# Optimization experiments

Hardware: AMD Instinct MI355X
Metric: run time of the kernel (lower is better)

The kernel has to match this reference:

```python
import jax, jax.numpy as jnp
import numpy as np

NUM_ITERS = 3
NUM_CAPSULES = 10
NUM_ROUTES = 1152  # 32*6*6
IN_CH = 16
OUT_CH = 32
BATCH = 128


def _squash(t):
    # Faithful to original squash(tensor) with default dim=1 (the batch axis here).
    n2 = jnp.sum(t * t, axis=1, keepdims=True)
    return (n2 / (1.0 + n2)) * t / jnp.sqrt(n2)


def setup_inputs() -> dict:
    key = jax.random.key(0)
    k1, k2 = jax.random.split(key)
    x = jax.random.normal(k1, (BATCH, NUM_ROUTES, IN_CH), dtype=jnp.float32)
    route_weights = jax.random.normal(
        k2, (NUM_CAPSULES, NUM_ROUTES, IN_CH, OUT_CH), dtype=jnp.float32)
    return {"x": x, "route_weights": route_weights}


def reference(x, route_weights):
    # prediction vectors u_hat: [C, B, R, O]
    pred = jnp.einsum('bri,crio->cbro', x, route_weights)
    logits = jnp.zeros_like(pred)  # [C, B, R, O], matching torch zeros of pred size
    outputs = None
    for i in range(NUM_ITERS):
        # routing_softmax with dim=2 -> softmax over the routes axis
        c = jax.nn.softmax(logits, axis=2)
        s = jnp.sum(c * pred, axis=2, keepdims=True)  # [C, B, 1, O]
        outputs = _squash(s)
        if i != NUM_ITERS - 1:
            # delta logits: [C, B, R, 1], broadcasts over O when added
            logits = logits + jnp.sum(pred * outputs, axis=-1, keepdims=True)
    # match torch output shape [C, B, 1, 1, O]
    return outputs[:, :, :, None, :]
```

## Files before the change

### kernel.cpp

```cpp
#include <hip/hip_runtime.h>
#include <math.h>

#define NB 128
#define NR 1152
#define NC 10
#define NCHK 24

typedef __attribute__((ext_vector_type(8))) short bf16x8;
typedef __attribute__((ext_vector_type(16))) float f32x16;

__device__ __forceinline__ unsigned pk_bf16(float a, float b) {
    unsigned r;
    asm("v_cvt_pk_bf16_f32 %0, %1, %2" : "=v"(r) : "v"(a), "v"(b));
    return r;
}

union UF { uint4 q; unsigned u[4]; bf16x8 v; };

template<int MODE>
__global__ __launch_bounds__(512, 2) void pass_z(const float* __restrict__ x,
                                                 const float* __restrict__ W,
                                                 unsigned* __restrict__ xts,
                                                 unsigned* __restrict__ wts,
                                                 float* __restrict__ oacc,
                                                 float* __restrict__ dout,
                                                 float* __restrict__ sbuf,
                                                 float* __restrict__ zbuf,
                                                 int* __restrict__ cnt)
{
    __shared__ float lds[16384];
    __shared__ int lastFlag;
    const int pb = blockIdx.x;
    const int lin = (pb & 7) * 30 + (pb >> 3);
    const int rch = lin / 10;
    const int c   = lin - rch * 10;
    const int t = threadIdx.x;
    const int w = t >> 6, l = t & 63;
    const int h = w >> 1, bp = w & 1;
    const int lo5 = l & 31, hi1 = l >> 5;
    const int r0 = rch * 48 + h * 12;

    if (MODE >= 1) {
        for (int idx = t; idx < 4096; idx += 512)
            lds[(idx >> 5) * 33 + (idx & 31)] = oacc[(size_t)c * 4096 + idx];
    }
    __syncthreads();

    float ov0[16], ov1[16];
    if (MODE >= 1) {
#pragma unroll
        for (int j = 0; j < 16; ++j) {
            int orow = (j & 3) + 8 * (j >> 2) + 4 * hi1;
            ov0[j] = lds[(bp * 64 + lo5) * 33 + orow];
            ov1[j] = lds[(bp * 64 + 32 + lo5) * 33 + orow];
        }
    }

    f32x16 acc0, acc1, zz;
#pragma unroll
    for (int j = 0; j < 16; ++j) { acc0[j] = 0.f; acc1[j] = 0.f; zz[j] = 0.f; }
    float Z0 = 0.f, Z1 = 0.f;

    const float* wb  = W + ((size_t)(c * NR + r0) * 16 + hi1 * 8) * 32 + lo5;
    const float* xp0 = x + ((size_t)(bp * 64 + lo5) * NR + r0) * 16 + hi1 * 8;
    const float* xp1 = x + ((size_t)(bp * 64 + 32 + lo5) * NR + r0) * 16 + hi1 * 8;
    uint4* xt4 = (uint4*)xts;
    uint4* wt4 = (uint4*)wts;
    const int bq0 = bp * 64 + lo5, bq1 = bq0 + 32;

#pragma unroll 4
    for (int rr = 0; rr < 12; ++rr) {
        UF Ah, Al, Xh0, Xl0, Xh1, Xl1;
        const size_t wrow = (size_t)(c * NR + r0 + rr) * 2;
        if (MODE == 0) {
            float wv[8];
#pragma unroll
            for (int j = 0; j < 8; ++j) wv[j] = wb[(size_t)rr * 512 + j * 32];
#pragma unroll
            for (int j = 0; j < 4; ++j) Ah.u[j] = pk_bf16(wv[2*j], wv[2*j+1]);
#pragma unroll
            for (int j = 0; j < 4; ++j) {
                float g0 = __uint_as_float(Ah.u[j] << 16);
                float g1 = __uint_as_float(Ah.u[j] & 0xffff0000u);
                Al.u[j] = pk_bf16(wv[2*j] - g0, wv[2*j+1] - g1);
            }
            if (bp == 0) {
                wt4[wrow * 64 + l]       = Ah.q;
                wt4[(wrow + 1) * 64 + l] = Al.q;
            }
        } else {
            Ah.q = wt4[wrow * 64 + l];
            Al.q = wt4[(wrow + 1) * 64 + l];
        }
        const size_t rb4 = ((size_t)((r0 + rr) * 2 + hi1) * 2) * 128;
        if (MODE == 0) {
            float4 u0 = *(const float4*)(xp0 + rr * 16);
            float4 u1 = *(const float4*)(xp0 + rr * 16 + 4);
            float4 v0 = *(const float4*)(xp1 + rr * 16);
            float4 v1 = *(const float4*)(xp1 + rr * 16 + 4);
            float xv0[8] = {u0.x,u0.y,u0.z,u0.w, u1.x,u1.y,u1.z,u1.w};
            float xv1[8] = {v0.x,v0.y,v0.z,v0.w, v1.x,v1.y,v1.z,v1.w};
#pragma unroll
            for (int j = 0; j < 4; ++j) Xh0.u[j] = pk_bf16(xv0[2*j], xv0[2*j+1]);
#pragma unroll
            for (int j = 0; j < 4; ++j) {
                float g0 = __uint_as_float(Xh0.u[j] << 16);
                float g1 = __uint_as_float(Xh0.u[j] & 0xffff0000u);
                Xl0.u[j] = pk_bf16(xv0[2*j] - g0, xv0[2*j+1] - g1);
            }
#pragma unroll
            for (int j = 0; j < 4; ++j) Xh1.u[j] = pk_bf16(xv1[2*j], xv1[2*j+1]);
#pragma unroll
            for (int j = 0; j < 4; ++j) {
                float g0 = __uint_as_float(Xh1.u[j] << 16);
                float g1 = __uint_as_float(Xh1.u[j] & 0xffff0000u);
                Xl1.u[j] = pk_bf16(xv1[2*j] - g0, xv1[2*j+1] - g1);
            }
            if (((h * 12 + rr) % 10) == c) {
                xt4[rb4 + bq0]       = Xh0.q;
                xt4[rb4 + 128 + bq0] = Xl0.q;
                xt4[rb4 + bq1]       = Xh1.q;
                xt4[rb4 + 128 + bq1] = Xl1.q;
            }
        } else {
            Xh0.q = xt4[rb4 + bq0];
            Xl0.q = xt4[rb4 + 128 + bq0];
            Xh1.q = xt4[rb4 + bq1];
            Xl1.q = xt4[rb4 + 128 + bq1];
        }

        if (MODE == 0) {
            acc0 = __builtin_amdgcn_mfma_f32_32x32x16_bf16(Ah.v, Xh0.v, acc0, 0, 0, 0);
            acc0 = __builtin_amdgcn_mfma_f32_32x32x16_bf16(Al.v, Xh0.v, acc0, 0, 0, 0);
            acc0 = __builtin_amdgcn_mfma_f32_32x32x16_bf16(Ah.v, Xl0.v, acc0, 0, 0, 0);
            acc1 = __builtin_amdgcn_mfma_f32_32x32x16_bf16(Ah.v, Xh1.v, acc1, 0, 0, 0);
            acc1 = __builtin_amdgcn_mfma_f32_32x32x16_bf16(Al.v, Xh1.v, acc1, 0, 0, 0);
            acc1 = __builtin_amdgcn_mfma_f32_32x32x16_bf16(Ah.v, Xl1.v, acc1, 0, 0, 0);
        } else {
            f32x16 q0, q1;
            q0 = __builtin_amdgcn_mfma_f32_32x32x16_bf16(Ah.v, Xh0.v, zz, 0, 0, 0);
            q1 = __builtin_amdgcn_mfma_f32_32x32x16_bf16(Ah.v, Xh1.v, zz, 0, 0, 0);
            q0 = __builtin_amdgcn_mfma_f32_32x32x16_bf16(Al.v, Xh0.v, q0, 0, 0, 0);
            q1 = __builtin_amdgcn_mfma_f32_32x32x16_bf16(Al.v, Xh1.v, q1, 0, 0, 0);
            q0 = __builtin_amdgcn_mfma_f32_32x32x16_bf16(Ah.v, Xl0.v, q0, 0, 0, 0);
            q1 = __builtin_amdgcn_mfma_f32_32x32x16_bf16(Ah.v, Xl1.v, q1, 0, 0, 0);
            float d0 = 0.f, d1 = 0.f;
#pragma unroll
            for (int j = 0; j < 16; ++j) {
                d0 = fmaf(q0[j], ov0[j], d0);
                d1 = fmaf(q1[j], ov1[j], d1);
            }
            d0 += __shfl_xor(d0, 32);
            d1 += __shfl_xor(d1, 32);
            float e0 = __expf(d0 - 20.0f);
            float e1 = __expf(d1 - 20.0f);
            Z0 += e0; Z1 += e1;
#pragma unroll
            for (int j = 0; j < 16; ++j) {
                acc0[j] = fmaf(e0, q0[j], acc0[j]);
                acc1[j] = fmaf(e1, q1[j], acc1[j]);
            }
        }
    }

    const int b0 = bp * 64 + lo5, b1 = b0 + 32;
    __syncthreads();
#pragma unroll
    for (int j = 0; j < 16; ++j) {
        int orow = (j & 3) + 8 * (j >> 2) + 4 * hi1;
        lds[h * 4096 + b0 * 32 + (orow ^ lo5)] = acc0[j];
        lds[h * 4096 + b1 * 32 + (orow ^ lo5)] = acc1[j];
    }
    __syncthreads();
    float* sc = sbuf + (size_t)c * 4096;
    for (int idx = t; idx < 4096; idx += 512) {
        int b = idx >> 5, o = idx & 31;
        float s = 0.f;
#pragma unroll
        for (int hh = 0; hh < 4; ++hh)
            s += lds[hh * 4096 + b * 32 + (o ^ (b & 31))];
        (void)__hip_atomic_fetch_add(sc + idx, s, __ATOMIC_RELAXED,
                                     __HIP_MEMORY_SCOPE_AGENT);
    }
    if (MODE >= 1) {
        __syncthreads();
        if (l < 32) {
            lds[h * 128 + bp * 64 + lo5] = Z0;
            lds[h * 128 + bp * 64 + 32 + lo5] = Z1;
        }
        __syncthreads();
        if (t < 128) {
            float z = lds[t] + lds[128 + t] + lds[256 + t] + lds[384 + t];
            (void)__hip_atomic_fetch_add(zbuf + (size_t)c * 128 + t, z,
                                         __ATOMIC_RELAXED, __HIP_MEMORY_SCOPE_AGENT);
        }
    }

    __syncthreads();
    if (t == 0) {
        int old = __hip_atomic_fetch_add(&cnt[c], 1,
                                         __ATOMIC_RELAXED, __HIP_MEMORY_SCOPE_AGENT);
        lastFlag = (old == NCHK - 1) ? 1 : 0;
    }
    __syncthreads();
    if (!lastFlag) return;

    if (MODE >= 1) {
        if (t < NB) {
            lds[8192 + t] = __hip_atomic_load(zbuf + (size_t)c * 128 + t,
                                              __ATOMIC_RELAXED, __HIP_MEMORY_SCOPE_AGENT);
        }
        __syncthreads();
    }
    float sv[8];
    float pn = 0.f;
#pragma unroll
    for (int k = 0; k < 8; ++k) {
        int idx = t + 512 * k;
        float s = __hip_atomic_load(sc + idx, __ATOMIC_RELAXED,
                                    __HIP_MEMORY_SCOPE_AGENT);
        float v = (MODE == 0) ? s * (1.0f / 1152.0f) : s / lds[8192 + (idx >> 5)];
        sv[k] = v;
        pn = fmaf(v, v, pn);
    }
    lds[(t >> 5) * 33 + (t & 31)] = pn;
    __syncthreads();
    if (t < 32) {
        float n2 = 0.f;
#pragma unroll
        for (int m = 0; m < 16; ++m) n2 += lds[m * 33 + t];
        lds[1024 + t] = sqrtf(n2) / (1.0f + n2);
    }
    __syncthreads();
    const float ff = lds[1024 + (t & 31)];
#pragma unroll
    for (int k = 0; k < 8; ++k) {
        int idx = t + 512 * k;
        float v = sv[k] * ff;
        if (MODE == 0)      oacc[(size_t)c * 4096 + idx] = v;
        else if (MODE == 1) oacc[(size_t)c * 4096 + idx] += v;
        else                dout[(size_t)c * 4096 + idx] = v;
    }
}

extern "C" void kernel_launch(void* const* d_in, const int* in_sizes, int n_in,
                              void* d_out, int out_size, void* d_ws, size_t ws_size,
                              hipStream_t stream)
{
    (void)in_sizes; (void)n_in; (void)out_size; (void)ws_size;
    const float* x = (const float*)d_in[0];
    const float* W = (const float*)d_in[1];
    float* wsf  = (float*)d_ws;
    float* outf = (float*)d_out;

    unsigned* xts = (unsigned*)d_ws;
    unsigned* wts = (unsigned*)d_ws + 2359296;
    float* sb   = wsf + 2359296 + 5898240;
    float* zb   = sb + 3 * 40960;
    int*   cnt  = (int*)(zb + 3 * 1280);
    float* oacc = (float*)(cnt + 32);

    hipMemsetAsync(sb, 0, (size_t)(3 * 40960 + 3 * 1280 + 32) * 4, stream);

    pass_z<0><<<240, 512, 0, stream>>>(x, W, xts, wts, oacc, nullptr,
                                       sb, zb, cnt);
    pass_z<1><<<240, 512, 0, stream>>>(x, W, xts, wts, oacc, nullptr,
                                       sb + 40960, zb + 1280, cnt + NC);
    pass_z<2><<<240, 512, 0, stream>>>(x, W, xts, wts, oacc, outf,
                                       sb + 2 * 40960, zb + 2 * 1280, cnt + 2 * NC);
}
```

Before: 66.65 us.

## Split batch across two blocks per chunk to double grid parallelism

```diff
diff --git a/kernel.cpp b/kernel.cpp
--- a/kernel.cpp
+++ b/kernel.cpp
@@ -4,7 +4,7 @@
 #define NB 128
 #define NR 1152
 #define NC 10
-#define NCHK 24
+#define NPC 48
 
 typedef __attribute__((ext_vector_type(8))) short bf16x8;
 typedef __attribute__((ext_vector_type(16))) float f32x16;
@@ -18,7 +18,7 @@
 union UF { uint4 q; unsigned u[4]; bf16x8 v; };
 
 template<int MODE>
-__global__ __launch_bounds__(512, 2) void pass_z(const float* __restrict__ x,
+__global__ __launch_bounds__(512, 2) void pass_w(const float* __restrict__ x,
                                                  const float* __restrict__ W,
                                                  unsigned* __restrict__ xts,
                                                  unsigned* __restrict__ wts,
@@ -31,46 +31,47 @@
     __shared__ float lds[16384];
     __shared__ int lastFlag;
     const int pb = blockIdx.x;
-    const int lin = (pb & 7) * 30 + (pb >> 3);
-    const int rch = lin / 10;
-    const int c   = lin - rch * 10;
+    const int lin = (pb & 7) * 60 + (pb >> 3);
+    const int c   = lin % 10;
+    const int g   = lin / 10;
+    const int bh  = g & 1;
+    const int rch = g >> 1;
     const int t = threadIdx.x;
     const int w = t >> 6, l = t & 63;
     const int h = w >> 1, bp = w & 1;
     const int lo5 = l & 31, hi1 = l >> 5;
     const int r0 = rch * 48 + h * 12;
+    const int bq = bh * 64 + bp * 32 + lo5;
 
     if (MODE >= 1) {
-        for (int idx = t; idx < 4096; idx += 512)
-            lds[(idx >> 5) * 33 + (idx & 31)] = oacc[(size_t)c * 4096 + idx];
-    }
-    __syncthreads();
-
-    float ov0[16], ov1[16];
+        for (int idx = t; idx < 2048; idx += 512)
+            lds[(idx >> 5) * 33 + (idx & 31)] =
+                oacc[(size_t)c * 4096 + bh * 2048 + idx];
+    }
+    __syncthreads();
+
+    float ov[16];
     if (MODE >= 1) {
 #pragma unroll
         for (int j = 0; j < 16; ++j) {
             int orow = (j & 3) + 8 * (j >> 2) + 4 * hi1;
-            ov0[j] = lds[(bp * 64 + lo5) * 33 + orow];
-            ov1[j] = lds[(bp * 64 + 32 + lo5) * 33 + orow];
-        }
-    }
-
-    f32x16 acc0, acc1, zz;
-#pragma unroll
-    for (int j = 0; j < 16; ++j) { acc0[j] = 0.f; acc1[j] = 0.f; zz[j] = 0.f; }
-    float Z0 = 0.f, Z1 = 0.f;
-
-    const float* wb  = W + ((size_t)(c * NR + r0) * 16 + hi1 * 8) * 32 + lo5;
-    const float* xp0 = x + ((size_t)(bp * 64 + lo5) * NR + r0) * 16 + hi1 * 8;
-    const float* xp1 = x + ((size_t)(bp * 64 + 32 + lo5) * NR + r0) * 16 + hi1 * 8;
+            ov[j] = lds[(bp * 32 + lo5) * 33 + orow];
+        }
+    }
+
+    f32x16 acc, zz;
+#pragma unroll
+    for (int j = 0; j < 16; ++j) { acc[j] = 0.f; zz[j] = 0.f; }
+    float Z = 0.f;
+
+    const float* wb = W + ((size_t)(c * NR + r0) * 16 + hi1 * 8) * 32 + lo5;
+    const float* xp = x + ((size_t)bq * NR + r0) * 16 + hi1 * 8;
     uint4* xt4 = (uint4*)xts;
     uint4* wt4 = (uint4*)wts;
-    const int bq0 = bp * 64 + lo5, bq1 = bq0 + 32;
 
 #pragma unroll 4
     for (int rr = 0; rr < 12; ++rr) {
-        UF Ah, Al, Xh0, Xl0, Xh1, Xl1;
+        UF Ah, Al, Xh, Xl;
         const size_t wrow = (size_t)(c * NR + r0 + rr) * 2;
         if (MODE == 0) {
             float wv[8];
@@ -84,7 +85,7 @@
                 float g1 = __uint_as_float(Ah.u[j] & 0xffff0000u);
                 Al.u[j] = pk_bf16(wv[2*j] - g0, wv[2*j+1] - g1);
             }
-            if (bp == 0) {
+            if (bh == 0 && bp == 0) {
                 wt4[wrow * 64 + l]       = Ah.q;
                 wt4[(wrow + 1) * 64 + l] = Al.q;
             }
@@ -94,113 +95,78 @@
         }
         const size_t rb4 = ((size_t)((r0 + rr) * 2 + hi1) * 2) * 128;
         if (MODE == 0) {
-            float4 u0 = *(const float4*)(xp0 + rr * 16);
-            float4 u1 = *(const float4*)(xp0 + rr * 16 + 4);
-            float4 v0 = *(const float4*)(xp1 + rr * 16);
-            float4 v1 = *(const float4*)(xp1 + rr * 16 + 4);
-            float xv0[8] = {u0.x,u0.y,u0.z,u0.w, u1.x,u1.y,u1.z,u1.w};
-            float xv1[8] = {v0.x,v0.y,v0.z,v0.w, v1.x,v1.y,v1.z,v1.w};
-#pragma unroll
-            for (int j = 0; j < 4; ++j) Xh0.u[j] = pk_bf16(xv0[2*j], xv0[2*j+1]);
+            float4 u0 = *(const float4*)(xp + rr * 16);
+            float4 u1 = *(const float4*)(xp + rr * 16 + 4);
+            float xv[8] = {u0.x,u0.y,u0.z,u0.w, u1.x,u1.y,u1.z,u1.w};
+#pragma unroll
+            for (int j = 0; j < 4; ++j) Xh.u[j] = pk_bf16(xv[2*j], xv[2*j+1]);
 #pragma unroll
             for (int j = 0; j < 4; ++j) {
-                float g0 = __uint_as_float(Xh0.u[j] << 16);
-                float g1 = __uint_as_float(Xh0.u[j] & 0xffff0000u);
-                Xl0.u[j] = pk_bf16(xv0[2*j] - g0, xv0[2*j+1] - g1);
-            }
-#pragma unroll
-            for (int j = 0; j < 4; ++j) Xh1.u[j] = pk_bf16(xv1[2*j], xv1[2*j+1]);
-#pragma unroll
-            for (int j = 0; j < 4; ++j) {
-                float g0 = __uint_as_float(Xh1.u[j] << 16);
-                float g1 = __uint_as_float(Xh1.u[j] & 0xffff0000u);
-                Xl1.u[j] = pk_bf16(xv1[2*j] - g0, xv1[2*j+1] - g1);
+                float g0 = __uint_as_float(Xh.u[j] << 16);
+                float g1 = __uint_as_float(Xh.u[j] & 0xffff0000u);
+                Xl.u[j] = pk_bf16(xv[2*j] - g0, xv[2*j+1] - g1);
             }
             if (((h * 12 + rr) % 10) == c) {
-                xt4[rb4 + bq0]       = Xh0.q;
-                xt4[rb4 + 128 + bq0] = Xl0.q;
-                xt4[rb4 + bq1]       = Xh1.q;
-                xt4[rb4 + 128 + bq1] = Xl1.q;
-            }
+                xt4[rb4 + bq]       = Xh.q;
+                xt4[rb4 + 128 + bq] = Xl.q;
+            }
+            acc = __builtin_amdgcn_mfma_f32_32x32x16_bf16(Ah.v, Xh.v, acc, 0, 0, 0);
+            acc = __builtin_amdgcn_mfma_f32_32x32x16_bf16(Al.v, Xh.v, acc, 0, 0, 0);
+            acc = __builtin_amdgcn_mfma_f32_32x32x16_bf16(Ah.v, Xl.v, acc, 0, 0, 0);
         } else {
-            Xh0.q = xt4[rb4 + bq0];
-            Xl0.q = xt4[rb4 + 128 + bq0];
-            Xh1.q = xt4[rb4 + bq1];
-            Xl1.q = xt4[rb4 + 128 + bq1];
-        }
-
-        if (MODE == 0) {
-            acc0 = __builtin_amdgcn_mfma_f32_32x32x16_bf16(Ah.v, Xh0.v, acc0, 0, 0, 0);
-            acc0 = __builtin_amdgcn_mfma_f32_32x32x16_bf16(Al.v, Xh0.v, acc0, 0, 0, 0);
-            acc0 = __builtin_amdgcn_mfma_f32_32x32x16_bf16(Ah.v, Xl0.v, acc0, 0, 0, 0);
-            acc1 = __builtin_amdgcn_mfma_f32_32x32x16_bf16(Ah.v, Xh1.v, acc1, 0, 0, 0);
-            acc1 = __builtin_amdgcn_mfma_f32_32x32x16_bf16(Al.v, Xh1.v, acc1, 0, 0, 0);
-            acc1 = __builtin_amdgcn_mfma_f32_32x32x16_bf16(Ah.v, Xl1.v, acc1, 0, 0, 0);
-        } else {
-            f32x16 q0, q1;
-            q0 = __builtin_amdgcn_mfma_f32_32x32x16_bf16(Ah.v, Xh0.v, zz, 0, 0, 0);
-            q1 = __builtin_amdgcn_mfma_f32_32x32x16_bf16(Ah.v, Xh1.v, zz, 0, 0, 0);
-            q0 = __builtin_amdgcn_mfma_f32_32x32x16_bf16(Al.v, Xh0.v, q0, 0, 0, 0);
-            q1 = __builtin_amdgcn_mfma_f32_32x32x16_bf16(Al.v, Xh1.v, q1, 0, 0, 0);
-            q0 = __builtin_amdgcn_mfma_f32_32x32x16_bf16(Ah.v, Xl0.v, q0, 0, 0, 0);
-            q1 = __builtin_amdgcn_mfma_f32_32x32x16_bf16(Ah.v, Xl1.v, q1, 0, 0, 0);
+            Xh.q = xt4[rb4 + bq];
+            Xl.q = xt4[rb4 + 128 + bq];
+            f32x16 q;
+            q = __builtin_amdgcn_mfma_f32_32x32x16_bf16(Ah.v, Xh.v, zz, 0, 0, 0);
+            q = __builtin_amdgcn_mfma_f32_32x32x16_bf16(Al.v, Xh.v, q, 0, 0, 0);
+            q = __builtin_amdgcn_mfma_f32_32x32x16_bf16(Ah.v, Xl.v, q, 0, 0, 0);
             float d0 = 0.f, d1 = 0.f;
 #pragma unroll
-            for (int j = 0; j < 16; ++j) {
-                d0 = fmaf(q0[j], ov0[j], d0);
-                d1 = fmaf(q1[j], ov1[j], d1);
-            }
-            d0 += __shfl_xor(d0, 32);
-            d1 += __shfl_xor(d1, 32);
-            float e0 = __expf(d0 - 20.0f);
-            float e1 = __expf(d1 - 20.0f);
-            Z0 += e0; Z1 += e1;
-#pragma unroll
-            for (int j = 0; j < 16; ++j) {
-                acc0[j] = fmaf(e0, q0[j], acc0[j]);
-                acc1[j] = fmaf(e1, q1[j], acc1[j]);
-            }
-        }
-    }
-
-    const int b0 = bp * 64 + lo5, b1 = b0 + 32;
+            for (int j = 0; j < 8; ++j) {
+                d0 = fmaf(q[2*j],   ov[2*j],   d0);
+                d1 = fmaf(q[2*j+1], ov[2*j+1], d1);
+            }
+            float d = d0 + d1;
+            d += __shfl_xor(d, 32);
+            float e = __expf(d - 20.0f);
+            Z += e;
+#pragma unroll
+            for (int j = 0; j < 16; ++j) acc[j] = fmaf(e, q[j], acc[j]);
+        }
+    }
+
+    const int bl = bp * 32 + lo5;
     __syncthreads();
 #pragma unroll
     for (int j = 0; j < 16; ++j) {
         int orow = (j & 3) + 8 * (j >> 2) + 4 * hi1;
-        lds[h * 4096 + b0 * 32 + (orow ^ lo5)] = acc0[j];
-        lds[h * 4096 + b1 * 32 + (orow ^ lo5)] = acc1[j];
-    }
+        lds[h * 2048 + bl * 32 + (orow ^ lo5)] = acc[j];
+    }
+    if (MODE >= 1 && l < 32) lds[8192 + h * 64 + bp * 32 + lo5] = Z;
     __syncthreads();
     float* sc = sbuf + (size_t)c * 4096;
-    for (int idx = t; idx < 4096; idx += 512) {
-        int b = idx >> 5, o = idx & 31;
+#pragma unroll
+    for (int k = 0; k < 4; ++k) {
+        int idx = t + 512 * k;
+        int b2 = idx >> 5, o = idx & 31;
         float s = 0.f;
 #pragma unroll
         for (int hh = 0; hh < 4; ++hh)
-            s += lds[hh * 4096 + b * 32 + (o ^ (b & 31))];
-        (void)__hip_atomic_fetch_add(sc + idx, s, __ATOMIC_RELAXED,
-                                     __HIP_MEMORY_SCOPE_AGENT);
-    }
-    if (MODE >= 1) {
-        __syncthreads();
-        if (l < 32) {
-            lds[h * 128 + bp * 64 + lo5] = Z0;
-            lds[h * 128 + bp * 64 + 32 + lo5] = Z1;
-        }
-        __syncthreads();
-        if (t < 128) {
-            float z = lds[t] + lds[128 + t] + lds[256 + t] + lds[384 + t];
-            (void)__hip_atomic_fetch_add(zbuf + (size_t)c * 128 + t, z,
-                                         __ATOMIC_RELAXED, __HIP_MEMORY_SCOPE_AGENT);
-        }
+            s += lds[hh * 2048 + b2 * 32 + (o ^ (b2 & 31))];
+        (void)__hip_atomic_fetch_add(sc + (size_t)(bh * 64 + b2) * 32 + o, s,
+                                     __ATOMIC_RELAXED, __HIP_MEMORY_SCOPE_AGENT);
+    }
+    if (MODE >= 1 && t < 64) {
+        float z = lds[8192 + t] + lds[8256 + t] + lds[8320 + t] + lds[8384 + t];
+        (void)__hip_atomic_fetch_add(zbuf + (size_t)c * 128 + bh * 64 + t, z,
+                                     __ATOMIC_RELAXED, __HIP_MEMORY_SCOPE_AGENT);
     }
 
     __syncthreads();
     if (t == 0) {
         int old = __hip_atomic_fetch_add(&cnt[c], 1,
                                          __ATOMIC_RELAXED, __HIP_MEMORY_SCOPE_AGENT);
-        lastFlag = (old == NCHK - 1) ? 1 : 0;
+        lastFlag = (old == NPC - 1) ? 1 : 0;
     }
     __syncthreads();
     if (!lastFlag) return;
@@ -262,10 +228,10 @@
 
     hipMemsetAsync(sb, 0, (size_t)(3 * 40960 + 3 * 1280 + 32) * 4, stream);
 
-    pass_z<0><<<240, 512, 0, stream>>>(x, W, xts, wts, oacc, nullptr,
+    pass_w<0><<<480, 512, 0, stream>>>(x, W, xts, wts, oacc, nullptr,
                                        sb, zb, cnt);
-    pass_z<1><<<240, 512, 0, stream>>>(x, W, xts, wts, oacc, nullptr,
+    pass_w<1><<<480, 512, 0, stream>>>(x, W, xts, wts, oacc, nullptr,
                                        sb + 40960, zb + 1280, cnt + NC);
-    pass_z<2><<<240, 512, 0, stream>>>(x, W, xts, wts, oacc, outf,
+    pass_w<2><<<480, 512, 0, stream>>>(x, W, xts, wts, oacc, outf,
                                        sb + 2 * 40960, zb + 2 * 1280, cnt + 2 * NC);
 }
```

Measured after the change: 72.30 us. 8.5% more time.
